# Performance work log

Hardware: AMD Instinct MI355X
Metric: run time of the kernel (lower is better)

Reference implementation:

```python
import jax, jax.numpy as jnp
import numpy as np

B, S, C = 64, 2048, 128
P, Q = 4, 4


def setup_inputs() -> dict:
    key = jax.random.key(0)
    k1, k2, k3 = jax.random.split(key, 3)
    y = jax.random.normal(k1, (B, S, C), dtype=jnp.float32)
    # small positive coefficients keep the MA recurrence stable over S steps
    phi = 0.1 * jax.random.uniform(k2, (P,), dtype=jnp.float32)
    theta = 0.1 * jax.random.uniform(k3, (Q,), dtype=jnp.float32)
    sigma2 = jnp.ones((1,), dtype=jnp.float32)
    return {"y": y, "phi": phi, "theta": theta, "sigma2": sigma2}


def reference(y, phi, theta, sigma2):
    # ARIMA negative log-likelihood (arima_log_likelihood):
    #   e_t = y_t - sum_i phi_i * y_{t-i-1} - sum_j theta_j * e_{t-j-1}
    #   nll = -[ -0.5*S*log(2*pi*sigma2) - 0.5*sum(e^2)/sigma2 ]
    b, s, c = y.shape
    p = phi.shape[0]
    q = theta.shape[0]

    # AR part is a fixed causal convolution over the input -> precompute, vectorized.
    ypad = jnp.pad(y, ((0, 0), (p, 0), (0, 0)))  # zeros for t-i-1 < 0
    # lags[i, :, t, :] = y[:, t-i-1, :]   (zero when out of range)
    lags = jnp.stack([ypad[:, p - 1 - i: p - 1 - i + s, :] for i in range(p)], axis=0)
    z = y - jnp.einsum('i,ibsc->bsc', phi, lags)  # (B,S,C)

    # MA part is a true recurrence on the errors -> lax.scan over time.
    def step(carry, z_t):
        # carry: (q, B, C) = [e_{t-1}, e_{t-2}, ..., e_{t-q}] (most recent first)
        ma = jnp.einsum('j,jbc->bc', theta, carry)
        e_t = z_t - ma
        carry = jnp.concatenate([e_t[None], carry[:-1]], axis=0)
        return carry, e_t

    e0 = jnp.zeros((q, b, c), dtype=z.dtype)
    _, e = jax.lax.scan(step, e0, jnp.swapaxes(z, 0, 1))  # e: (S,B,C)

    ll = -0.5 * s * jnp.log(2.0 * jnp.pi * sigma2) - 0.5 * jnp.sum(e * e) / sigma2
    return -ll  # shape (1,)
```

## Files before the change

### kernel.cpp

```cpp
#include <hip/hip_runtime.h>
#include <math.h>

#define BB   64
#define SS   2048
#define CC   128
#define LCH  256
#define NCH  (SS / LCH)
#define WARM 64
#define UNR  16

#define ARIMA_STEP(SRC, ACCT)                                          \
    _Pragma("unroll")                                                  \
    for (int j = 0; j < UNR; ++j) {                                    \
        const float y0 = SRC[j];                                       \
        const float z  = y0 - p1*y1 - p2*y2 - p3*y3 - p4*y4;           \
        const float e0 = z  - q1*e1 - q2*e2 - q3*e3 - q4*e4;           \
        if (ACCT) acc += e0 * e0;                                      \
        y4 = y3; y3 = y2; y2 = y1; y1 = y0;                            \
        e4 = e3; e3 = e2; e2 = e1; e1 = e0;                            \
    }

__global__ __launch_bounds__(CC) void arima_main(
    const float* __restrict__ y,
    const float* __restrict__ phi,
    const float* __restrict__ theta,
    float* __restrict__ partials)
{
    const int bidx  = blockIdx.x;
    const int b     = bidx >> 3;
    const int chunk = bidx & 7;
    const int c     = threadIdx.x;

    const float p1 = phi[0],   p2 = phi[1],   p3 = phi[2],   p4 = phi[3];
    const float q1 = theta[0], q2 = theta[1], q3 = theta[2], q4 = theta[3];

    const float* base = y + (size_t)b * SS * CC + c;

    const int start = chunk * LCH;
    const int warm  = chunk ? WARM : 0;
    const int t0    = start - warm;
    const int total = warm + LCH;
    const int nblk  = total / UNR;
    const int wblk  = warm / UNR;

    float y1 = 0.f, y2 = 0.f, y3 = 0.f, y4 = 0.f;
    if (chunk) {
        y1 = base[(size_t)(t0 - 1) * CC];
        y2 = base[(size_t)(t0 - 2) * CC];
        y3 = base[(size_t)(t0 - 3) * CC];
        y4 = base[(size_t)(t0 - 4) * CC];
    }
    float e1 = 0.f, e2 = 0.f, e3 = 0.f, e4 = 0.f;
    float acc = 0.f;

    const float* p = base + (size_t)t0 * CC;
    float cur[UNR];
#pragma unroll
    for (int j = 0; j < UNR; ++j) cur[j] = p[(size_t)j * CC];
    p += (size_t)UNR * CC;

    for (int blk = 0; blk < nblk - 1; ++blk) {
        float nxt[UNR];
#pragma unroll
        for (int j = 0; j < UNR; ++j) nxt[j] = p[(size_t)j * CC];
        p += (size_t)UNR * CC;
        const bool acct = (blk >= wblk);
        ARIMA_STEP(cur, acct)
#pragma unroll
        for (int j = 0; j < UNR; ++j) cur[j] = nxt[j];
    }
    ARIMA_STEP(cur, true)

#pragma unroll
    for (int off = 32; off > 0; off >>= 1)
        acc += __shfl_down(acc, off, 64);
    __shared__ float sw[2];
    if ((threadIdx.x & 63) == 0) sw[threadIdx.x >> 6] = acc;
    __syncthreads();
    if (threadIdx.x == 0) partials[bidx] = sw[0] + sw[1];
}

__global__ __launch_bounds__(512) void arima_final(
    const float* __restrict__ partials,
    const float* __restrict__ sigma2,
    float* __restrict__ out)
{
    float v = partials[threadIdx.x];
#pragma unroll
    for (int off = 32; off > 0; off >>= 1)
        v += __shfl_down(v, off, 64);
    __shared__ float sw[8];
    if ((threadIdx.x & 63) == 0) sw[threadIdx.x >> 6] = v;
    __syncthreads();
    if (threadIdx.x == 0) {
        float tot = 0.f;
#pragma unroll
        for (int i = 0; i < 8; ++i) tot += sw[i];
        const float s2 = sigma2[0];
        out[0] = 0.5f * (float)SS * logf(2.0f * 3.14159265358979323846f * s2)
               + 0.5f * tot / s2;
    }
}

extern "C" void kernel_launch(void* const* d_in, const int* in_sizes, int n_in,
                              void* d_out, int out_size, void* d_ws, size_t ws_size,
                              hipStream_t stream) {
    const float* y      = (const float*)d_in[0];
    const float* phi    = (const float*)d_in[1];
    const float* theta  = (const float*)d_in[2];
    const float* sigma2 = (const float*)d_in[3];
    float* out      = (float*)d_out;
    float* partials = (float*)d_ws;

    arima_main<<<BB * NCH, CC, 0, stream>>>(y, phi, theta, partials);
    arima_final<<<1, 512, 0, stream>>>(partials, sigma2, out);
}
```

Before: 104.7 us.

## Use float4 channel loads, shorter time chunks, and two chunks per wavefront

Each thread now handles four channels through float4 loads. The time axis is split into 32 chunks of 64 steps with a 32-step warm-up, and each 64-lane block holds two chunks, so the block-level shared reduction is no longer needed. This gives four independent recurrences per thread for ILP and wider memory transactions, which targets the latency-bound serial recurrence. In exchange the redundant warm-up work grows relative to the chunk length (32 on 64), and the shorter warm-up relies on fast decay of the MA state to stay accurate.

```diff
diff --git a/kernel.cpp b/kernel.cpp
--- a/kernel.cpp
+++ b/kernel.cpp
@@ -4,98 +4,112 @@
 #define BB   64
 #define SS   2048
 #define CC   128
-#define LCH  256
+#define C4   (CC / 4)
+#define LCH  64
 #define NCH  (SS / LCH)
-#define WARM 64
+#define WARM 32
 #define UNR  16
+#define STEPS (WARM + LCH)
+#define NBLK  (STEPS / UNR)
+#define WBLK  (WARM / UNR)
 
-#define ARIMA_STEP(SRC, ACCT)                                          \
-    _Pragma("unroll")                                                  \
-    for (int j = 0; j < UNR; ++j) {                                    \
-        const float y0 = SRC[j];                                       \
-        const float z  = y0 - p1*y1 - p2*y2 - p3*y3 - p4*y4;           \
-        const float e0 = z  - q1*e1 - q2*e2 - q3*e3 - q4*e4;           \
-        if (ACCT) acc += e0 * e0;                                      \
-        y4 = y3; y3 = y2; y2 = y1; y1 = y0;                            \
-        e4 = e3; e3 = e2; e2 = e1; e1 = e0;                            \
+#define ARIMA_BATCH(SRC, ACCT)                                            \
+    _Pragma("unroll")                                                     \
+    for (int j = 0; j < UNR; ++j) {                                       \
+        _Pragma("unroll")                                                 \
+        for (int k = 0; k < 4; ++k) {                                     \
+            const float y0 = SRC[j][k];                                   \
+            const float z  = y0 - p1*Y1[k] - p2*Y2[k] - p3*Y3[k] - p4*Y4[k]; \
+            const float e0 = z  - q2*E2[k] - q3*E3[k] - q4*E4[k] - q1*E1[k]; \
+            if (ACCT) acc[k] += e0 * e0;                                  \
+            Y4[k] = Y3[k]; Y3[k] = Y2[k]; Y2[k] = Y1[k]; Y1[k] = y0;      \
+            E4[k] = E3[k]; E3[k] = E2[k]; E2[k] = E1[k]; E1[k] = e0;      \
+        }                                                                 \
     }
 
-__global__ __launch_bounds__(CC) void arima_main(
-    const float* __restrict__ y,
+__global__ __launch_bounds__(64) void arima_main(
+    const float4* __restrict__ yv,
     const float* __restrict__ phi,
     const float* __restrict__ theta,
     float* __restrict__ partials)
 {
-    const int bidx  = blockIdx.x;
-    const int b     = bidx >> 3;
-    const int chunk = bidx & 7;
-    const int c     = threadIdx.x;
+    const int bid  = blockIdx.x;
+    const int lane = threadIdx.x;
+    const int grp  = lane >> 5;
+    const int ch   = lane & 31;
+    const int b    = bid >> 4;
+    const int chunk = ((bid & 15) << 1) | grp;
 
     const float p1 = phi[0],   p2 = phi[1],   p3 = phi[2],   p4 = phi[3];
     const float q1 = theta[0], q2 = theta[1], q3 = theta[2], q4 = theta[3];
 
-    const float* base = y + (size_t)b * SS * CC + c;
+    const float4* base = yv + (size_t)b * SS * C4 + ch;
+    const int t0 = chunk * LCH - WARM;
 
-    const int start = chunk * LCH;
-    const int warm  = chunk ? WARM : 0;
-    const int t0    = start - warm;
-    const int total = warm + LCH;
-    const int nblk  = total / UNR;
-    const int wblk  = warm / UNR;
+    float Y1[4] = {0,0,0,0}, Y2[4] = {0,0,0,0}, Y3[4] = {0,0,0,0}, Y4[4] = {0,0,0,0};
+    if (t0 >= 4) {
+        float4 v;
+        v = base[(size_t)(t0-1) * C4]; Y1[0]=v.x; Y1[1]=v.y; Y1[2]=v.z; Y1[3]=v.w;
+        v = base[(size_t)(t0-2) * C4]; Y2[0]=v.x; Y2[1]=v.y; Y2[2]=v.z; Y2[3]=v.w;
+        v = base[(size_t)(t0-3) * C4]; Y3[0]=v.x; Y3[1]=v.y; Y3[2]=v.z; Y3[3]=v.w;
+        v = base[(size_t)(t0-4) * C4]; Y4[0]=v.x; Y4[1]=v.y; Y4[2]=v.z; Y4[3]=v.w;
+    }
+    float E1[4] = {0,0,0,0}, E2[4] = {0,0,0,0}, E3[4] = {0,0,0,0}, E4[4] = {0,0,0,0};
+    float acc[4] = {0,0,0,0};
 
-    float y1 = 0.f, y2 = 0.f, y3 = 0.f, y4 = 0.f;
-    if (chunk) {
-        y1 = base[(size_t)(t0 - 1) * CC];
-        y2 = base[(size_t)(t0 - 2) * CC];
-        y3 = base[(size_t)(t0 - 3) * CC];
-        y4 = base[(size_t)(t0 - 4) * CC];
+    int tcur = t0;
+    float cur[UNR][4];
+#pragma unroll
+    for (int j = 0; j < UNR; ++j) {
+        const int t = tcur + j;
+        float4 v = (t >= 0) ? base[(size_t)t * C4] : make_float4(0.f,0.f,0.f,0.f);
+        cur[j][0]=v.x; cur[j][1]=v.y; cur[j][2]=v.z; cur[j][3]=v.w;
     }
-    float e1 = 0.f, e2 = 0.f, e3 = 0.f, e4 = 0.f;
-    float acc = 0.f;
+    tcur += UNR;
 
-    const float* p = base + (size_t)t0 * CC;
-    float cur[UNR];
+    for (int blk = 0; blk < NBLK - 1; ++blk) {
+        float nxt[UNR][4];
 #pragma unroll
-    for (int j = 0; j < UNR; ++j) cur[j] = p[(size_t)j * CC];
-    p += (size_t)UNR * CC;
+        for (int j = 0; j < UNR; ++j) {
+            const int t = tcur + j;
+            float4 v = (t >= 0) ? base[(size_t)t * C4] : make_float4(0.f,0.f,0.f,0.f);
+            nxt[j][0]=v.x; nxt[j][1]=v.y; nxt[j][2]=v.z; nxt[j][3]=v.w;
+        }
+        tcur += UNR;
+        const bool acct = (blk >= WBLK);
+        ARIMA_BATCH(cur, acct)
+#pragma unroll
+        for (int j = 0; j < UNR; ++j) {
+            cur[j][0]=nxt[j][0]; cur[j][1]=nxt[j][1];
+            cur[j][2]=nxt[j][2]; cur[j][3]=nxt[j][3];
+        }
+    }
+    ARIMA_BATCH(cur, true)
 
-    for (int blk = 0; blk < nblk - 1; ++blk) {
-        float nxt[UNR];
-#pragma unroll
-        for (int j = 0; j < UNR; ++j) nxt[j] = p[(size_t)j * CC];
-        p += (size_t)UNR * CC;
-        const bool acct = (blk >= wblk);
-        ARIMA_STEP(cur, acct)
-#pragma unroll
-        for (int j = 0; j < UNR; ++j) cur[j] = nxt[j];
-    }
-    ARIMA_STEP(cur, true)
-
+    float a = acc[0] + acc[1] + acc[2] + acc[3];
 #pragma unroll
     for (int off = 32; off > 0; off >>= 1)
-        acc += __shfl_down(acc, off, 64);
-    __shared__ float sw[2];
-    if ((threadIdx.x & 63) == 0) sw[threadIdx.x >> 6] = acc;
-    __syncthreads();
-    if (threadIdx.x == 0) partials[bidx] = sw[0] + sw[1];
+        a += __shfl_down(a, off, 64);
+    if (lane == 0) partials[bid] = a;
 }
 
-__global__ __launch_bounds__(512) void arima_final(
+__global__ __launch_bounds__(256) void arima_final(
     const float* __restrict__ partials,
     const float* __restrict__ sigma2,
     float* __restrict__ out)
 {
-    float v = partials[threadIdx.x];
+    float v = 0.f;
+#pragma unroll
+    for (int i = 0; i < 4; ++i)
+        v += partials[threadIdx.x + 256 * i];
 #pragma unroll
     for (int off = 32; off > 0; off >>= 1)
         v += __shfl_down(v, off, 64);
-    __shared__ float sw[8];
+    __shared__ float sw[4];
     if ((threadIdx.x & 63) == 0) sw[threadIdx.x >> 6] = v;
     __syncthreads();
     if (threadIdx.x == 0) {
-        float tot = 0.f;
-#pragma unroll
-        for (int i = 0; i < 8; ++i) tot += sw[i];
+        const float tot = sw[0] + sw[1] + sw[2] + sw[3];
         const float s2 = sigma2[0];
         out[0] = 0.5f * (float)SS * logf(2.0f * 3.14159265358979323846f * s2)
                + 0.5f * tot / s2;
@@ -105,13 +119,13 @@
 extern "C" void kernel_launch(void* const* d_in, const int* in_sizes, int n_in,
                               void* d_out, int out_size, void* d_ws, size_t ws_size,
                               hipStream_t stream) {
-    const float* y      = (const float*)d_in[0];
+    const float4* yv    = (const float4*)d_in[0];
     const float* phi    = (const float*)d_in[1];
     const float* theta  = (const float*)d_in[2];
     const float* sigma2 = (const float*)d_in[3];
     float* out      = (float*)d_out;
     float* partials = (float*)d_ws;
 
-    arima_main<<<BB * NCH, CC, 0, stream>>>(y, phi, theta, partials);
-    arima_final<<<1, 512, 0, stream>>>(partials, sigma2, out);
+    arima_main<<<BB * NCH / 2, 64, 0, stream>>>(yv, phi, theta, partials);
+    arima_final<<<1, 256, 0, stream>>>(partials, sigma2, out);
 }
```

Result: faster. 101.9 us (-2.7%).
